# Performance work log

Measured on AMD Instinct MI355X. Metric: run time of the kernel, lower is better.

## Reference

```python
import jax, jax.numpy as jnp
import numpy as np

B, NPG, EPG = 128, 256, 2048   # graphs, nodes/graph, edges/graph
EMB, EH, L = 256, 64, 5
ATOM_V, BOND_V = 119, 16


def setup_inputs() -> dict:
    key = jax.random.key(0)
    ks = iter(jax.random.split(key, 32))
    s = 0.02
    inp = {
        'atom_idx': jax.random.randint(next(ks), (B, NPG), 0, ATOM_V),
        'local_edge_index': jax.random.randint(next(ks), (B, 2, EPG), 0, NPG),
        'edge_attr_idx': jax.random.randint(next(ks), (B, EPG), 0, BOND_V),
        'order': 3,
        'atom_emb': jax.random.normal(next(ks), (ATOM_V, EMB), jnp.float32) * s,
        'bond_emb_h': jax.random.normal(next(ks), (BOND_V, EH), jnp.float32) * s,
        'edge_lin_w': jax.random.normal(next(ks), (EH,), jnp.float32) * s,
        'edge_lin_b': jax.random.normal(next(ks), (1,), jnp.float32) * s,
        'bond_emb_l': jax.random.normal(next(ks), (L, BOND_V, EMB), jnp.float32) * s,
        'gin_eps': jnp.zeros((L,), jnp.float32),
        'mlp_w1': jax.random.normal(next(ks), (L, EMB, 2 * EMB), jnp.float32) * s,
        'mlp_b1': jax.random.normal(next(ks), (L, 2 * EMB), jnp.float32) * s,
        'mlp_bn_g': jnp.ones((L, 2 * EMB), jnp.float32),
        'mlp_bn_b': jnp.zeros((L, 2 * EMB), jnp.float32),
        'mlp_w2': jax.random.normal(next(ks), (L, 2 * EMB, EMB), jnp.float32) * s,
        'mlp_b2': jax.random.normal(next(ks), (L, EMB), jnp.float32) * s,
        'out_bn_g': jnp.ones((L, EMB), jnp.float32),
        'out_bn_b': jnp.zeros((L, EMB), jnp.float32),
        'vn_emb': jnp.zeros((1, EMB), jnp.float32),  # init constant 0 as in source
        'vn_w1': jax.random.normal(next(ks), (L - 1, EMB, 2 * EMB), jnp.float32) * s,
        'vn_b1': jax.random.normal(next(ks), (L - 1, 2 * EMB), jnp.float32) * s,
        'vn_w2': jax.random.normal(next(ks), (L - 1, 2 * EMB, EMB), jnp.float32) * s,
        'vn_b2': jax.random.normal(next(ks), (L - 1, EMB), jnp.float32) * s,
    }
    return inp


def _batchnorm(x, g, b):
    # training-mode BN math (biased variance), eps=1e-5 as in torch.nn.BatchNorm1d
    mu = x.mean(0)
    var = ((x - mu) ** 2).mean(0)
    return (x - mu) * jax.lax.rsqrt(var + 1e-5) * g + b


def reference(atom_idx, local_edge_index, edge_attr_idx, order,
              atom_emb, bond_emb_h, edge_lin_w, edge_lin_b, bond_emb_l, gin_eps,
              mlp_w1, mlp_b1, mlp_bn_g, mlp_bn_b, mlp_w2, mlp_b2,
              out_bn_g, out_bn_b, vn_emb, vn_w1, vn_b1, vn_w2, vn_b2):
    Bg, n = atom_idx.shape
    emb = atom_emb.shape[1]
    N = Bg * n
    nl = gin_eps.shape[0]

    # ---- per-graph learned-adjacency dense propagation (adj_learn=1) ----
    fea = atom_emb[atom_idx]                                       # [B,n,emb]
    ew = jax.nn.sigmoid(jnp.einsum('beh,h->be', bond_emb_h[edge_attr_idx], edge_lin_w)
                        + edge_lin_b[0])                           # [B,e]

    def per_graph(f, ei, w):
        adj = jnp.zeros((n, n), f.dtype).at[ei[0], ei[1]].set(w)
        adj = adj + jnp.eye(n, dtype=f.dtype)
        # A = diag(colsum^-1/2) @ adj @ diag(rowsum^-1/2)  (as in source naming)
        r_row = adj.sum(0) ** -0.5
        r_col = adj.sum(1) ** -0.5
        A = r_row[:, None] * adj * r_col[None, :]
        x = f
        y = f
        for _ in range(order):
            x = A @ x
            y = y + x
        return y / (order + 1.0)

    h = jax.vmap(per_graph)(fea, local_edge_index, ew).reshape(N, emb)

    # ---- flatten batched graph to global edge list ----
    batch = jnp.repeat(jnp.arange(Bg), n)                          # [N]
    off = (jnp.arange(Bg) * n)[:, None]
    src = (local_edge_index[:, 0] + off).reshape(-1)               # [E]
    dst = (local_edge_index[:, 1] + off).reshape(-1)
    ea = edge_attr_idx.reshape(-1)

    # ---- virtual-node GIN stack (eval: dropout = identity) ----
    vn = jnp.broadcast_to(vn_emb[0], (Bg, emb))
    for l in range(nl):
        h = h + vn[batch]
        h_in = h
        eemb = bond_emb_l[l][ea]                                   # [E,emb]
        msg = jax.nn.relu(h[src] + eemb)
        agg = jax.ops.segment_sum(msg, dst, num_segments=N)
        z = (1.0 + gin_eps[l]) * h + agg
        z = _batchnorm(z @ mlp_w1[l] + mlp_b1[l], mlp_bn_g[l], mlp_bn_b[l])
        z = jax.nn.relu(z) @ mlp_w2[l] + mlp_b2[l]
        z = _batchnorm(z, out_bn_g[l], out_bn_b[l])
        if l < nl - 1:
            z = jax.nn.relu(z)
            vt = jax.ops.segment_sum(h_in, batch, num_segments=Bg) + vn
            vn = jax.nn.relu(jax.nn.relu(vt @ vn_w1[l] + vn_b1[l]) @ vn_w2[l] + vn_b2[l])
        h = z
    return h  # JK='last'
```

## Files before the change

### kernel.cpp

```cpp
#include <hip/hip_runtime.h>
#include <math.h>


#define B_G   128
#define NPG   256
#define EPG   2048
#define EMB   256
#define NL    5
#define NNODE (B_G*NPG)
#define NEDGE (B_G*EPG)
#define FBUF  8388608

typedef __attribute__((ext_vector_type(8))) short bf16x8;
typedef __attribute__((ext_vector_type(4))) float f32x4;

__device__ __forceinline__ unsigned short round1(float x) {
  unsigned u = __builtin_bit_cast(unsigned, x);
  return (unsigned short)((u + 0x7FFFu + ((u >> 16) & 1u)) >> 16);
}

__device__ __forceinline__ float bdec(unsigned short h) {
  return __builtin_bit_cast(float, (unsigned)h << 16);
}

__device__ __forceinline__ void gload16(unsigned short* lds, const unsigned short* g) {
  __builtin_amdgcn_global_load_lds(
      (const __attribute__((address_space(1))) unsigned int*)g,
      (__attribute__((address_space(3))) unsigned int*)lds, 16, 0, 0);
}

__global__ void k_zero(uint4* p, int n16) {
  int i = blockIdx.x * 256 + threadIdx.x;
  if (i < n16) p[i] = make_uint4(0, 0, 0, 0);
}

__global__ void k_ewtbl(const float* __restrict__ bh, const float* __restrict__ w,
                        const float* __restrict__ b, float* __restrict__ tbl) {
  int v = threadIdx.x >> 6, t = threadIdx.x & 63;
  float p = bh[v * 64 + t] * w[t];
  for (int off = 32; off; off >>= 1) p += __shfl_down(p, off, 64);
  if (t == 0) tbl[v] = 1.0f / (1.0f + expf(-(p + b[0])));
}

__global__ void k_pack_adj(const int* __restrict__ lei, const int* __restrict__ ea,
                           int* __restrict__ packed) {
  int idx = blockIdx.x * 256 + threadIdx.x;
  int g = idx >> 11, e = idx & 2047;
  int s = lei[g * 4096 + e];
  int d = lei[g * 4096 + 2048 + e];
  int v = ((e + 1) << 4) | ea[g * 2048 + e];
  atomicMax(&packed[g * 65536 + s * 256 + d], v);
}

__global__ void k_unpack_adj(const int* __restrict__ packed,
                             const float* __restrict__ tbl, float* __restrict__ adj) {
  int idx = blockIdx.x * 256 + threadIdx.x;
  int v = packed[idx];
  int r = (idx >> 8) & 255, c = idx & 255;
  adj[idx] = (v ? tbl[v & 15] : 0.0f) + (r == c ? 1.0f : 0.0f);
}

__global__ __launch_bounds__(256)
void k_degsums(const float* __restrict__ adj, float* __restrict__ CSv,
               float* __restrict__ RCv) {
  int g = blockIdx.x, t = threadIdx.x;
  const float* Ag = adj + (size_t)g * 65536;
  float s0 = 0, s1 = 0, s2 = 0, s3 = 0;
  for (int i = 0; i < 256; i += 4) {
    s0 += Ag[(i + 0) * 256 + t]; s1 += Ag[(i + 1) * 256 + t];
    s2 += Ag[(i + 2) * 256 + t]; s3 += Ag[(i + 3) * 256 + t];
  }
  CSv[g * 256 + t] = rsqrtf((s0 + s1) + (s2 + s3));
  float4 r0 = make_float4(0, 0, 0, 0), r1 = r0, r2 = r0, r3 = r0;
  const float4* A4 = (const float4*)(Ag + t * 256);
  for (int j = 0; j < 64; j += 4) {
    float4 v0 = A4[j], v1 = A4[j + 1], v2 = A4[j + 2], v3 = A4[j + 3];
    r0.x += v0.x + v0.y; r0.y += v0.z + v0.w;
    r1.x += v1.x + v1.y; r1.y += v1.z + v1.w;
    r2.x += v2.x + v2.y; r2.y += v2.z + v2.w;
    r3.x += v3.x + v3.y; r3.y += v3.z + v3.w;
  }
  RCv[g * 256 + t] = rsqrtf((r0.x + r0.y) + (r1.x + r1.y) + (r2.x + r2.y) + (r3.x + r3.y));
}

__global__ void k_ascale(const float* __restrict__ adj, const float* __restrict__ CSv,
                         const float* __restrict__ RCv, unsigned short* __restrict__ Ahb) {
  int flat = blockIdx.x * 256 + threadIdx.x;
  int g = flat >> 14;
  int i = (flat >> 6) & 255, j4 = (flat & 63) * 4;
  size_t base = (size_t)g * 65536 + i * 256 + j4;
  float4 a = *(const float4*)&adj[base];
  float cs = CSv[g * 256 + i];
  float4 rc = *(const float4*)&RCv[g * 256 + j4];
  ushort4 o;
  o.x = round1(cs * a.x * rc.x); o.y = round1(cs * a.y * rc.y);
  o.z = round1(cs * a.z * rc.z); o.w = round1(cs * a.w * rc.w);
  *(ushort4*)&Ahb[base] = o;
}

__global__ void k_feaTb(const int* __restrict__ aidx, const float* __restrict__ aemb,
                        unsigned short* __restrict__ X0h) {
  int flat = blockIdx.x * 256 + threadIdx.x;
  int base = flat * 4;
  int g = base >> 16, e = (base >> 8) & 255, n0 = base & 255;
  const int* ai = &aidx[g * 256 + n0];
  ushort4 o;
  o.x = round1(aemb[ai[0] * 256 + e]);
  o.y = round1(aemb[ai[1] * 256 + e]);
  o.z = round1(aemb[ai[2] * 256 + e]);
  o.w = round1(aemb[ai[3] * 256 + e]);
  *(ushort4*)&X0h[base] = o;
}

__global__ __launch_bounds__(256)
void k_sumT(const unsigned short* __restrict__ X0, const unsigned short* __restrict__ X1,
            const unsigned short* __restrict__ X2, const unsigned short* __restrict__ X3,
            unsigned short* __restrict__ dst) {
  __shared__ float tl[64][65];
  size_t zo = (size_t)blockIdx.z * 65536;
  int n0 = blockIdx.x * 64, k0 = blockIdx.y * 64;
  int t = threadIdx.x;
  int c = (t & 15) * 4, r = t >> 4;
#pragma unroll
  for (int p = 0; p < 4; p++) {
    int rr = r + p * 16;
    size_t off = zo + (size_t)(k0 + rr) * 256 + n0 + c;
    ushort4 a = *(const ushort4*)&X0[off];
    ushort4 b = *(const ushort4*)&X1[off];
    ushort4 cc = *(const ushort4*)&X2[off];
    ushort4 d = *(const ushort4*)&X3[off];
    tl[rr][c + 0] = bdec(a.x) + bdec(b.x) + bdec(cc.x) + bdec(d.x);
    tl[rr][c + 1] = bdec(a.y) + bdec(b.y) + bdec(cc.y) + bdec(d.y);
    tl[rr][c + 2] = bdec(a.z) + bdec(b.z) + bdec(cc.z) + bdec(d.z);
    tl[rr][c + 3] = bdec(a.w) + bdec(b.w) + bdec(cc.w) + bdec(d.w);
  }
  __syncthreads();
#pragma unroll
  for (int p = 0; p < 4; p++) {
    int rr = r + p * 16;
    ushort4 o;
    o.x = round1(tl[c][rr] * 0.25f);     o.y = round1(tl[c + 1][rr] * 0.25f);
    o.z = round1(tl[c + 2][rr] * 0.25f); o.w = round1(tl[c + 3][rr] * 0.25f);
    *(ushort4*)&dst[zo + (size_t)(n0 + rr) * 256 + k0 + c] = o;
  }
}

__global__ __launch_bounds__(256)
void k_wtb(const float* __restrict__ src, unsigned short* __restrict__ dh,
           int K, int N, long ss, long sd) {
  __shared__ float tl[64][65];
  src += (size_t)blockIdx.z * ss;
  dh += (size_t)blockIdx.z * sd;
  int n0 = blockIdx.x * 64, k0 = blockIdx.y * 64;
  int t = threadIdx.x;
  int c = (t & 15) * 4, r = t >> 4;
#pragma unroll
  for (int p = 0; p < 4; p++) {
    int rr = r + p * 16;
    float4 v = *(const float4*)&src[(size_t)(k0 + rr) * N + n0 + c];
    tl[rr][c] = v.x; tl[rr][c + 1] = v.y; tl[rr][c + 2] = v.z; tl[rr][c + 3] = v.w;
  }
  __syncthreads();
#pragma unroll
  for (int p = 0; p < 4; p++) {
    int rr = r + p * 16;
    ushort4 hh;
    hh.x = round1(tl[c][rr]);     hh.y = round1(tl[c + 1][rr]);
    hh.z = round1(tl[c + 2][rr]); hh.w = round1(tl[c + 3][rr]);
    *(ushort4*)&dh[(size_t)(n0 + rr) * K + k0 + c] = hh;
  }
}

__global__ __launch_bounds__(256, 4)
void k_bgemm(const unsigned short* __restrict__ A_g, const unsigned short* __restrict__ B_g,
             const float* __restrict__ bias, float* __restrict__ Cf,
             unsigned short* __restrict__ Ch,
             float* __restrict__ Ssum, float* __restrict__ Ssq, int K, int N,
             long zA, long zB, long zC) {
  __shared__ alignas(16) unsigned short As[128 * 64];
  __shared__ alignas(16) unsigned short Bs[128 * 64];
  int z = blockIdx.z;
  A_g += (size_t)z * zA; B_g += (size_t)z * zB;
  if (Cf) Cf += (size_t)z * zC;
  if (Ch) Ch += (size_t)z * zC;
  int rowbase = blockIdx.y * 128, colbase = blockIdx.x * 128;
  int t = threadIdx.x, l = t & 63, wid = t >> 6;
  int wr = wid >> 1, wc = wid & 1;
  int r8 = l >> 3, cb = (l & 7) * 8;
  f32x4 acc[4][4];
#pragma unroll
  for (int i = 0; i < 4; i++)
#pragma unroll
    for (int j = 0; j < 4; j++) acc[i][j] = (f32x4){0, 0, 0, 0};

  for (int k0 = 0; k0 < K; k0 += 64) {
    __syncthreads();
#pragma unroll
    for (int i = 0; i < 4; i++) {
      int chunk = wid * 4 + i;
      int row = chunk * 8 + r8;
      gload16(As + chunk * 512, A_g + (size_t)(rowbase + row) * K + k0 + cb);
      gload16(Bs + chunk * 512, B_g + (size_t)(colbase + row) * K + k0 + cb);
    }
    __syncthreads();
#pragma unroll
    for (int ks = 0; ks < 2; ks++) {
      bf16x8 ah[4], bh[4];
#pragma unroll
      for (int fm = 0; fm < 4; fm++) {
        int r = wr * 64 + fm * 16 + (l & 15);
        ah[fm] = *(const bf16x8*)&As[r * 64 + ks * 32 + (l >> 4) * 8];
      }
#pragma unroll
      for (int fn = 0; fn < 4; fn++) {
        int c = wc * 64 + fn * 16 + (l & 15);
        bh[fn] = *(const bf16x8*)&Bs[c * 64 + ks * 32 + (l >> 4) * 8];
      }
#pragma unroll
      for (int fm = 0; fm < 4; fm++)
#pragma unroll
        for (int fn = 0; fn < 4; fn++)
          acc[fm][fn] = __builtin_amdgcn_mfma_f32_16x16x32_bf16(ah[fm], bh[fn], acc[fm][fn], 0, 0, 0);
    }
  }
  __syncthreads();
  float bi[4], scoll[4] = {0, 0, 0, 0}, qcoll[4] = {0, 0, 0, 0};
#pragma unroll
  for (int fn = 0; fn < 4; fn++)
    bi[fn] = bias ? bias[colbase + wc * 64 + fn * 16 + (l & 15)] : 0.0f;
#pragma unroll
  for (int fm = 0; fm < 4; fm++)
#pragma unroll
    for (int r4 = 0; r4 < 4; r4++) {
      int row = rowbase + wr * 64 + fm * 16 + (l >> 4) * 4 + r4;
#pragma unroll
      for (int fn = 0; fn < 4; fn++) {
        int col = colbase + wc * 64 + fn * 16 + (l & 15);
        float v = acc[fm][fn][r4] + bi[fn];
        size_t idx = (size_t)row * N + col;
        if (Cf) Cf[idx] = v;
        if (Ch) Ch[idx] = round1(v);
        scoll[fn] += v; qcoll[fn] += v * v;
      }
    }
  if (Ssum) {
    float* scr = (float*)As;
    scr[t] = 0.0f;
    __syncthreads();
#pragma unroll
    for (int fn = 0; fn < 4; fn++) {
      int cl_ = wc * 64 + fn * 16 + (l & 15);
      atomicAdd(&scr[cl_ * 2], scoll[fn]);
      atomicAdd(&scr[cl_ * 2 + 1], qcoll[fn]);
    }
    __syncthreads();
    if (t < 128) {
      atomicAdd(&Ssum[colbase + t], scr[t * 2]);
      atomicAdd(&Ssq[colbase + t], scr[t * 2 + 1]);
    }
  }
}

__global__ void k_bnsplit(unsigned short* __restrict__ Th,
                          const float* __restrict__ Ssum, const float* __restrict__ Ssq,
                          const float* __restrict__ g, const float* __restrict__ b) {
  size_t i = (size_t)blockIdx.x * 256 + threadIdx.x;
  int c4 = ((int)i & 127) * 4;
  ushort4 h4 = *(ushort4*)&Th[i * 4];
  float4 ss = *(const float4*)&Ssum[c4], qq = *(const float4*)&Ssq[c4];
  float4 gg = *(const float4*)&g[c4],    bb = *(const float4*)&b[c4];
  const float invN = 1.0f / 32768.0f;
  float x, mu, var, sc, sh;
#define BNS(cmp) \
  mu = ss.cmp * invN; var = qq.cmp * invN - mu * mu; \
  sc = rsqrtf(var + 1e-5f) * gg.cmp; sh = bb.cmp - mu * sc; \
  x = bdec(h4.cmp); x = fmaf(x, sc, sh); x = x > 0 ? x : 0; \
  h4.cmp = round1(x);
  BNS(x) BNS(y) BNS(z) BNS(w)
#undef BNS
  *(ushort4*)&Th[i * 4] = h4;
}

__global__ void k_count(const int* __restrict__ lei, int* __restrict__ counts) {
  int idx = blockIdx.x * 256 + threadIdx.x;
  int g = idx >> 11, e = idx & 2047;
  int d = lei[g * 4096 + 2048 + e];
  atomicAdd(&counts[g * 256 + d], 1);
}

__global__ void k_scan(const int* __restrict__ counts, int* __restrict__ rowptr,
                       int* __restrict__ pos) {
  int g = blockIdx.x, t = threadIdx.x;
  __shared__ int sc[256];
  int own = counts[g * 256 + t];
  sc[t] = own;
  __syncthreads();
  for (int off = 1; off < 256; off <<= 1) {
    int v = 0;
    if (t >= off) v = sc[t - off];
    __syncthreads();
    sc[t] += v;
    __syncthreads();
  }
  int val = g * 2048 + sc[t] - own;
  rowptr[g * 256 + t] = val;
  pos[g * 256 + t] = val;
  if (g == B_G - 1 && t == 255) rowptr[B_G * 256] = B_G * 2048;
}

__global__ void k_fill(const int* __restrict__ lei, const int* __restrict__ ea,
                       int* __restrict__ pos, int* __restrict__ csr) {
  int idx = blockIdx.x * 256 + threadIdx.x;
  int g = idx >> 11, e = idx & 2047;
  int s = lei[g * 4096 + e];
  int d = lei[g * 4096 + 2048 + e];
  int eav = ea[g * 2048 + e];
  int slot = atomicAdd(&pos[g * 256 + d], 1);
  csr[slot] = s | (eav << 16);
}

__global__ __launch_bounds__(256)
void k_agg(const unsigned short* __restrict__ H,
           const float* __restrict__ hsc, const float* __restrict__ hsh,
           const float* __restrict__ vn, int vns,
           const float* __restrict__ eemb,
           const int* __restrict__ rowptr, const int* __restrict__ csr,
           const float* __restrict__ geps, int l,
           unsigned short* __restrict__ Zh) {
  __shared__ float ee[16 * 256];
  for (int i = threadIdx.x; i < 4096; i += 256) ee[i] = eemb[i];
  __syncthreads();
  int lane = threadIdx.x & 63, w = threadIdx.x >> 6;
  int bid = (blockIdx.x & 7) * 1024 + (blockIdx.x >> 3);
  int m = bid * 4 + w;
  int g = m >> 8;
  int d = lane * 4;
  float eps1 = 1.0f + geps[l];
  float4 sc4 = make_float4(0, 0, 0, 0), sh4 = make_float4(0, 0, 0, 0);
  if (hsc) { sc4 = *(const float4*)&hsc[d]; sh4 = *(const float4*)&hsh[d]; }
  float4 vn4 = *(const float4*)&vn[(size_t)g * vns + d];
  int rp = rowptr[m], rp1 = rowptr[m + 1];
  float4 acc = make_float4(0, 0, 0, 0);
  int gbase = g << 8;
  for (int j = rp; j < rp1; j++) {
    int cw = csr[j];
    int src = cw & 0xFFFF, eav = cw >> 16;
    ushort4 hr = *(const ushort4*)&H[(size_t)(gbase + src) * 256 + d];
    float4 h4 = make_float4(bdec(hr.x), bdec(hr.y), bdec(hr.z), bdec(hr.w));
    if (hsc) {
      h4.x = fmaf(h4.x, sc4.x, sh4.x); h4.y = fmaf(h4.y, sc4.y, sh4.y);
      h4.z = fmaf(h4.z, sc4.z, sh4.z); h4.w = fmaf(h4.w, sc4.w, sh4.w);
      h4.x = h4.x > 0 ? h4.x : 0; h4.y = h4.y > 0 ? h4.y : 0;
      h4.z = h4.z > 0 ? h4.z : 0; h4.w = h4.w > 0 ? h4.w : 0;
    }
    const float4 e4 = *(const float4*)&ee[eav * 256 + d];
    float mx = h4.x + vn4.x + e4.x; float my = h4.y + vn4.y + e4.y;
    float mz = h4.z + vn4.z + e4.z; float mw = h4.w + vn4.w + e4.w;
    acc.x += mx > 0 ? mx : 0; acc.y += my > 0 ? my : 0;
    acc.z += mz > 0 ? mz : 0; acc.w += mw > 0 ? mw : 0;
  }
  ushort4 hsr = *(const ushort4*)&H[(size_t)m * 256 + d];
  float4 hs = make_float4(bdec(hsr.x), bdec(hsr.y), bdec(hsr.z), bdec(hsr.w));
  if (hsc) {
    hs.x = fmaf(hs.x, sc4.x, sh4.x); hs.y = fmaf(hs.y, sc4.y, sh4.y);
    hs.z = fmaf(hs.z, sc4.z, sh4.z); hs.w = fmaf(hs.w, sc4.w, sh4.w);
    hs.x = hs.x > 0 ? hs.x : 0; hs.y = hs.y > 0 ? hs.y : 0;
    hs.z = hs.z > 0 ? hs.z : 0; hs.w = hs.w > 0 ? hs.w : 0;
  }
  float4 z4;
  z4.x = eps1 * (hs.x + vn4.x) + acc.x;
  z4.y = eps1 * (hs.y + vn4.y) + acc.y;
  z4.z = eps1 * (hs.z + vn4.z) + acc.z;
  z4.w = eps1 * (hs.w + vn4.w) + acc.w;
  ushort4 hh;
  hh.x = round1(z4.x); hh.y = round1(z4.y);
  hh.z = round1(z4.z); hh.w = round1(z4.w);
  *(ushort4*)&Zh[(size_t)m * 256 + d] = hh;
}

__global__ __launch_bounds__(256)
void k_vnsum(const unsigned short* __restrict__ H,
             const float* __restrict__ hsc, const float* __restrict__ hsh,
             float* __restrict__ VNP) {
  int g = blockIdx.x >> 1, p = blockIdx.x & 1, t = threadIdx.x;
  float sc = 0, sh = 0;
  if (hsc) { sc = hsc[t]; sh = hsh[t]; }
  int base = g * 256 + p * 128;
  float s0 = 0, s1 = 0, s2 = 0, s3 = 0;
  for (int i = 0; i < 128; i += 4) {
    float v0 = bdec(H[(size_t)(base + i + 0) * 256 + t]);
    float v1 = bdec(H[(size_t)(base + i + 1) * 256 + t]);
    float v2 = bdec(H[(size_t)(base + i + 2) * 256 + t]);
    float v3 = bdec(H[(size_t)(base + i + 3) * 256 + t]);
    if (hsc) {
      v0 = fmaf(v0, sc, sh); v0 = v0 > 0 ? v0 : 0;
      v1 = fmaf(v1, sc, sh); v1 = v1 > 0 ? v1 : 0;
      v2 = fmaf(v2, sc, sh); v2 = v2 > 0 ? v2 : 0;
      v3 = fmaf(v3, sc, sh); v3 = v3 > 0 ? v3 : 0;
    }
    s0 += v0; s1 += v1; s2 += v2; s3 += v3;
  }
  VNP[(size_t)(p * 128 + g) * 256 + t] = (s0 + s1) + (s2 + s3);
}

__global__ __launch_bounds__(256)
void k_vn(const float* __restrict__ VNP,
          const float* __restrict__ vn_in, int vns,
          const float* __restrict__ W1, const float* __restrict__ B1,
          const float* __restrict__ W2, const float* __restrict__ B2,
          float* __restrict__ vn_out) {
  int g = blockIdx.x, t = threadIdx.x;
  __shared__ float vt[256];
  __shared__ float u[512];
  vt[t] = VNP[(size_t)g * 256 + t] + VNP[(size_t)(128 + g) * 256 + t]
        + 257.0f * vn_in[(size_t)g * vns + t];
  __syncthreads();
  for (int o = t; o < 512; o += 256) {
    float a = B1[o];
    for (int k = 0; k < 256; k++) a = fmaf(vt[k], W1[k * 512 + o], a);
    u[o] = a > 0 ? a : 0;
  }
  __syncthreads();
  float a = B2[t];
  for (int k = 0; k < 512; k++) a = fmaf(u[k], W2[k * 256 + t], a);
  vn_out[g * 256 + t] = a > 0 ? a : 0;
}

__global__ void k_bnfin(const float* __restrict__ Ssum, const float* __restrict__ Ssq,
                        const float* __restrict__ g, const float* __restrict__ b,
                        float* __restrict__ scale, float* __restrict__ shift,
                        int NC, float invN) {
  int c = blockIdx.x * 256 + threadIdx.x;
  if (c >= NC) return;
  float mu = Ssum[c] * invN;
  float var = Ssq[c] * invN - mu * mu;
  float rs = rsqrtf(var + 1e-5f);
  float s = rs * g[c];
  scale[c] = s;
  shift[c] = b[c] - mu * s;
}

__global__ void k_final(const float* __restrict__ T2, const float* __restrict__ sc,
                        const float* __restrict__ sh, float* __restrict__ out) {
  int i = blockIdx.x * 256 + threadIdx.x;
  int c4 = (i & 63) * 4;
  float4 v = *(const float4*)&T2[(size_t)i * 4];
  float4 s4 = *(const float4*)&sc[c4];
  float4 h4 = *(const float4*)&sh[c4];
  v.x = fmaf(v.x, s4.x, h4.x); v.y = fmaf(v.y, s4.y, h4.y);
  v.z = fmaf(v.z, s4.z, h4.z); v.w = fmaf(v.w, s4.w, h4.w);
  *(float4*)&out[(size_t)i * 4] = v;
}

extern "C" void kernel_launch(void* const* d_in, const int* in_sizes, int n_in,
                              void* d_out, int out_size, void* d_ws, size_t ws_size,
                              hipStream_t stream) {
  (void)in_sizes; (void)n_in; (void)out_size; (void)ws_size;
  const int*   atom_idx = (const int*)d_in[0];
  const int*   lei      = (const int*)d_in[1];
  const int*   eattr    = (const int*)d_in[2];
  const float* atom_emb = (const float*)d_in[4];
  const float* bemb_h   = (const float*)d_in[5];
  const float* elw      = (const float*)d_in[6];
  const float* elb      = (const float*)d_in[7];
  const float* bemb_l   = (const float*)d_in[8];
  const float* geps     = (const float*)d_in[9];
  const float* mw1      = (const float*)d_in[10];
  const float* mb1      = (const float*)d_in[11];
  const float* mbng     = (const float*)d_in[12];
  const float* mbnb     = (const float*)d_in[13];
  const float* mw2      = (const float*)d_in[14];
  const float* mb2      = (const float*)d_in[15];
  const float* obng     = (const float*)d_in[16];
  const float* obnb     = (const float*)d_in[17];
  const float* vne      = (const float*)d_in[18];
  const float* vw1      = (const float*)d_in[19];
  const float* vb1      = (const float*)d_in[20];
  const float* vw2      = (const float*)d_in[21];
  const float* vb2      = (const float*)d_in[22];
  float* out = (float*)d_out;

  float* W   = (float*)d_ws;
  float* A_  = W;
  float* U1  = W + (size_t)FBUF;
  float* U2  = W + (size_t)2 * FBUF;
  float* U3  = W + (size_t)3 * FBUF;
  float* Z_  = W + (size_t)4 * FBUF;
  float* SM  = W + (size_t)5 * FBUF;
  float* EWT = SM;
  float* S1S = SM + 256;
  float* S1Q = SM + 768;
  float* S2S = SM + 1280;
  float* S2Q = SM + 1536;
  float* SC2 = SM + 1792;
  float* SH2 = SM + 2048;
  float* VNA = SM + 2304;
  float* VNB = SM + 35072;
  float* CSv = SM + 67840;
  float* RCv = SM + 100608;
  int* ROWPTR = (int*)(SM + 133376);
  int* POS    = ROWPTR + 32772;
  int* COUNTS = POS + 32768;
  int* CSR    = COUNTS + 32768;
  unsigned short* W1hT = (unsigned short*)(SM + 493952);
  unsigned short* W2hT = (unsigned short*)(SM + 821632);
  float* T2f = A_;
  unsigned short* T2b = (unsigned short*)A_;
  unsigned short* H0b = (unsigned short*)U3;
  int* PACKED = (int*)U3;
  unsigned short* X0h = (unsigned short*)U1;
  unsigned short* X1h = X0h + 8388608;
  unsigned short* X2h = (unsigned short*)U2;
  unsigned short* X3h = X2h + 8388608;
  unsigned short* T1h = (unsigned short*)U1;
  unsigned short* Zh  = (unsigned short*)Z_;
  unsigned short* Ahb = (unsigned short*)(Z_ + (size_t)FBUF / 2);
  float* VNP  = (float*)POS;

  k_zero<<<8192, 256, 0, stream>>>((uint4*)PACKED, 2097152);
  k_zero<<<32, 256, 0, stream>>>((uint4*)COUNTS, 8192);
  k_ewtbl<<<1, 1024, 0, stream>>>(bemb_h, elw, elb, EWT);
  k_pack_adj<<<NEDGE / 256, 256, 0, stream>>>(lei, eattr, PACKED);
  k_unpack_adj<<<32768, 256, 0, stream>>>(PACKED, EWT, A_);
  k_degsums<<<B_G, 256, 0, stream>>>(A_, CSv, RCv);
  k_ascale<<<8192, 256, 0, stream>>>(A_, CSv, RCv, Ahb);
  k_wtb<<<dim3(8, 4, 5), 256, 0, stream>>>(mw1, W1hT, 256, 512, 131072, 131072);
  k_wtb<<<dim3(4, 8, 5), 256, 0, stream>>>(mw2, W2hT, 512, 256, 131072, 131072);
  k_feaTb<<<8192, 256, 0, stream>>>(atom_idx, atom_emb, X0h);
  k_bgemm<<<dim3(2, 2, B_G), 256, 0, stream>>>(X0h, Ahb, nullptr, nullptr, X1h,
      nullptr, nullptr, 256, 256, 65536, 65536, 65536);
  k_bgemm<<<dim3(2, 2, B_G), 256, 0, stream>>>(X1h, Ahb, nullptr, nullptr, X2h,
      nullptr, nullptr, 256, 256, 65536, 65536, 65536);
  k_bgemm<<<dim3(2, 2, B_G), 256, 0, stream>>>(X2h, Ahb, nullptr, nullptr, X3h,
      nullptr, nullptr, 256, 256, 65536, 65536, 65536);
  k_sumT<<<dim3(4, 4, B_G), 256, 0, stream>>>(X0h, X1h, X2h, X3h, H0b);

  k_count<<<NEDGE / 256, 256, 0, stream>>>(lei, COUNTS);
  k_scan<<<B_G, 256, 0, stream>>>(COUNTS, ROWPTR, POS);
  k_fill<<<NEDGE / 256, 256, 0, stream>>>(lei, eattr, POS, CSR);

  const float* vn_cur = vne; int vns = 0;
  float* vn_next = VNA;
  for (int l = 0; l < NL; l++) {
    const unsigned short* hsrc = (l == 0) ? H0b : T2b;
    const float* hsc  = (l == 0) ? nullptr : SC2;
    const float* hsh  = (l == 0) ? nullptr : SH2;
    k_agg<<<NNODE / 4, 256, 0, stream>>>(hsrc, hsc, hsh, vn_cur, vns,
        bemb_l + (size_t)l * 16 * EMB, ROWPTR, CSR, geps, l, Zh);
    if (l < NL - 1) {
      k_vnsum<<<256, 256, 0, stream>>>(hsrc, hsc, hsh, VNP);
      k_vn<<<B_G, 256, 0, stream>>>(VNP, vn_cur, vns,
          vw1 + (size_t)l * EMB * 512, vb1 + (size_t)l * 512,
          vw2 + (size_t)l * 512 * EMB, vb2 + (size_t)l * EMB, vn_next);
    }
    k_zero<<<2, 256, 0, stream>>>((uint4*)S1S, 384);
    k_bgemm<<<dim3(4, 256, 1), 256, 0, stream>>>(Zh,
        W1hT + (size_t)l * 131072, mb1 + (size_t)l * 512,
        nullptr, T1h, S1S, S1Q, 256, 512, 0, 0, 0);
    k_bnsplit<<<16384, 256, 0, stream>>>(T1h, S1S, S1Q,
        mbng + (size_t)l * 512, mbnb + (size_t)l * 512);
    if (l < NL - 1)
      k_bgemm<<<dim3(2, 256, 1), 256, 0, stream>>>(T1h,
          W2hT + (size_t)l * 131072, mb2 + (size_t)l * 256,
          nullptr, T2b, S2S, S2Q, 512, 256, 0, 0, 0);
    else
      k_bgemm<<<dim3(2, 256, 1), 256, 0, stream>>>(T1h,
          W2hT + (size_t)l * 131072, mb2 + (size_t)l * 256,
          T2f, nullptr, S2S, S2Q, 512, 256, 0, 0, 0);
    k_bnfin<<<1, 256, 0, stream>>>(S2S, S2Q, obng + (size_t)l * EMB,
        obnb + (size_t)l * EMB, SC2, SH2, 256, 1.0f / NNODE);
    if (l < NL - 1) {
      vn_cur = vn_next; vns = EMB;
      vn_next = (vn_next == VNA) ? VNB : VNA;
    }
  }
  k_final<<<8192, 256, 0, stream>>>(T2f, SC2, SH2, out);
}
```

Measured before the change: 1.028 ms.

## Fuse BN+ReLU into second MLP GEMM A-load; restructure aggregation with prefetch

Removes the standalone k_bnsplit pass. The first-layer BN scale and shift are now computed by k_bnfin, and BN plus ReLU is applied while loading A tiles into shared memory in the second GEMM. This avoids a full read-modify-write of the 32768x512 bf16 intermediate on every layer. The aggregation kernel now processes four nodes per wave with a one-ahead software prefetch of the CSR entry and neighbour row, and stores the edge embeddings as bf16 in LDS. The costs are a synchronous (non-async) A-load path in the GEMM, an extra bf16 rounding of the edge embeddings, and fewer blocks for the aggregation.

```diff
diff --git a/kernel.cpp b/kernel.cpp
--- a/kernel.cpp
+++ b/kernel.cpp
@@ -176,7 +176,8 @@
              const float* __restrict__ bias, float* __restrict__ Cf,
              unsigned short* __restrict__ Ch,
              float* __restrict__ Ssum, float* __restrict__ Ssq, int K, int N,
-             long zA, long zB, long zC) {
+             long zA, long zB, long zC,
+             const float* __restrict__ ascale, const float* __restrict__ ashift) {
   __shared__ alignas(16) unsigned short As[128 * 64];
   __shared__ alignas(16) unsigned short Bs[128 * 64];
   int z = blockIdx.z;
@@ -195,12 +196,38 @@
 
   for (int k0 = 0; k0 < K; k0 += 64) {
     __syncthreads();
-#pragma unroll
-    for (int i = 0; i < 4; i++) {
-      int chunk = wid * 4 + i;
-      int row = chunk * 8 + r8;
-      gload16(As + chunk * 512, A_g + (size_t)(rowbase + row) * K + k0 + cb);
-      gload16(Bs + chunk * 512, B_g + (size_t)(colbase + row) * K + k0 + cb);
+    if (ascale) {
+      float4 s0 = *(const float4*)&ascale[k0 + cb];
+      float4 s1 = *(const float4*)&ascale[k0 + cb + 4];
+      float4 h0 = *(const float4*)&ashift[k0 + cb];
+      float4 h1 = *(const float4*)&ashift[k0 + cb + 4];
+#pragma unroll
+      for (int i = 0; i < 4; i++) {
+        int chunk = wid * 4 + i;
+        int row = chunk * 8 + r8;
+        const unsigned short* src = A_g + (size_t)(rowbase + row) * K + k0 + cb;
+        ushort4 v0 = *(const ushort4*)src;
+        ushort4 v1 = *(const ushort4*)(src + 4);
+        float x;
+        ushort4 o0, o1;
+#define BNF(dst, u, s, h) x = fmaf(bdec(u), s, h); x = x > 0 ? x : 0; dst = round1(x);
+        BNF(o0.x, v0.x, s0.x, h0.x) BNF(o0.y, v0.y, s0.y, h0.y)
+        BNF(o0.z, v0.z, s0.z, h0.z) BNF(o0.w, v0.w, s0.w, h0.w)
+        BNF(o1.x, v1.x, s1.x, h1.x) BNF(o1.y, v1.y, s1.y, h1.y)
+        BNF(o1.z, v1.z, s1.z, h1.z) BNF(o1.w, v1.w, s1.w, h1.w)
+#undef BNF
+        *(ushort4*)&As[chunk * 512 + l * 8] = o0;
+        *(ushort4*)&As[chunk * 512 + l * 8 + 4] = o1;
+        gload16(Bs + chunk * 512, B_g + (size_t)(colbase + row) * K + k0 + cb);
+      }
+    } else {
+#pragma unroll
+      for (int i = 0; i < 4; i++) {
+        int chunk = wid * 4 + i;
+        int row = chunk * 8 + r8;
+        gload16(As + chunk * 512, A_g + (size_t)(rowbase + row) * K + k0 + cb);
+        gload16(Bs + chunk * 512, B_g + (size_t)(colbase + row) * K + k0 + cb);
+      }
     }
     __syncthreads();
 #pragma unroll
@@ -259,26 +286,6 @@
       atomicAdd(&Ssq[colbase + t], scr[t * 2 + 1]);
     }
   }
-}
-
-__global__ void k_bnsplit(unsigned short* __restrict__ Th,
-                          const float* __restrict__ Ssum, const float* __restrict__ Ssq,
-                          const float* __restrict__ g, const float* __restrict__ b) {
-  size_t i = (size_t)blockIdx.x * 256 + threadIdx.x;
-  int c4 = ((int)i & 127) * 4;
-  ushort4 h4 = *(ushort4*)&Th[i * 4];
-  float4 ss = *(const float4*)&Ssum[c4], qq = *(const float4*)&Ssq[c4];
-  float4 gg = *(const float4*)&g[c4],    bb = *(const float4*)&b[c4];
-  const float invN = 1.0f / 32768.0f;
-  float x, mu, var, sc, sh;
-#define BNS(cmp) \
-  mu = ss.cmp * invN; var = qq.cmp * invN - mu * mu; \
-  sc = rsqrtf(var + 1e-5f) * gg.cmp; sh = bb.cmp - mu * sc; \
-  x = bdec(h4.cmp); x = fmaf(x, sc, sh); x = x > 0 ? x : 0; \
-  h4.cmp = round1(x);
-  BNS(x) BNS(y) BNS(z) BNS(w)
-#undef BNS
-  *(ushort4*)&Th[i * 4] = h4;
 }
 
 __global__ void k_count(const int* __restrict__ lei, int* __restrict__ counts) {
@@ -327,55 +334,67 @@
            const int* __restrict__ rowptr, const int* __restrict__ csr,
            const float* __restrict__ geps, int l,
            unsigned short* __restrict__ Zh) {
-  __shared__ float ee[16 * 256];
-  for (int i = threadIdx.x; i < 4096; i += 256) ee[i] = eemb[i];
+  __shared__ unsigned short ee[16 * 256];
+  for (int i = threadIdx.x; i < 4096; i += 256) ee[i] = round1(eemb[i]);
   __syncthreads();
   int lane = threadIdx.x & 63, w = threadIdx.x >> 6;
-  int bid = (blockIdx.x & 7) * 1024 + (blockIdx.x >> 3);
-  int m = bid * 4 + w;
-  int g = m >> 8;
+  int bid = (blockIdx.x & 7) * 256 + (blockIdx.x >> 3);
+  int g = bid >> 4;
   int d = lane * 4;
   float eps1 = 1.0f + geps[l];
   float4 sc4 = make_float4(0, 0, 0, 0), sh4 = make_float4(0, 0, 0, 0);
   if (hsc) { sc4 = *(const float4*)&hsc[d]; sh4 = *(const float4*)&hsh[d]; }
   float4 vn4 = *(const float4*)&vn[(size_t)g * vns + d];
-  int rp = rowptr[m], rp1 = rowptr[m + 1];
-  float4 acc = make_float4(0, 0, 0, 0);
   int gbase = g << 8;
-  for (int j = rp; j < rp1; j++) {
-    int cw = csr[j];
-    int src = cw & 0xFFFF, eav = cw >> 16;
-    ushort4 hr = *(const ushort4*)&H[(size_t)(gbase + src) * 256 + d];
-    float4 h4 = make_float4(bdec(hr.x), bdec(hr.y), bdec(hr.z), bdec(hr.w));
+#pragma unroll 1
+  for (int mi = 0; mi < 4; mi++) {
+    int m = bid * 16 + w * 4 + mi;
+    int rp = rowptr[m], rp1 = rowptr[m + 1];
+    ushort4 hsr = *(const ushort4*)&H[(size_t)m * 256 + d];
+    float4 acc = make_float4(0, 0, 0, 0);
+    int cw = 0; ushort4 hr = make_ushort4(0, 0, 0, 0);
+    if (rp < rp1) {
+      cw = csr[rp];
+      hr = *(const ushort4*)&H[(size_t)(gbase + (cw & 0xFFFF)) * 256 + d];
+    }
+    for (int j = rp; j < rp1; j++) {
+      int cwn = 0; ushort4 hrn = make_ushort4(0, 0, 0, 0);
+      if (j + 1 < rp1) {
+        cwn = csr[j + 1];
+        hrn = *(const ushort4*)&H[(size_t)(gbase + (cwn & 0xFFFF)) * 256 + d];
+      }
+      int eav = cw >> 16;
+      float4 h4 = make_float4(bdec(hr.x), bdec(hr.y), bdec(hr.z), bdec(hr.w));
+      if (hsc) {
+        h4.x = fmaf(h4.x, sc4.x, sh4.x); h4.y = fmaf(h4.y, sc4.y, sh4.y);
+        h4.z = fmaf(h4.z, sc4.z, sh4.z); h4.w = fmaf(h4.w, sc4.w, sh4.w);
+        h4.x = h4.x > 0 ? h4.x : 0; h4.y = h4.y > 0 ? h4.y : 0;
+        h4.z = h4.z > 0 ? h4.z : 0; h4.w = h4.w > 0 ? h4.w : 0;
+      }
+      const ushort4 er = *(const ushort4*)&ee[eav * 256 + d];
+      float mx = h4.x + vn4.x + bdec(er.x); float my = h4.y + vn4.y + bdec(er.y);
+      float mz = h4.z + vn4.z + bdec(er.z); float mw = h4.w + vn4.w + bdec(er.w);
+      acc.x += mx > 0 ? mx : 0; acc.y += my > 0 ? my : 0;
+      acc.z += mz > 0 ? mz : 0; acc.w += mw > 0 ? mw : 0;
+      cw = cwn; hr = hrn;
+    }
+    float4 hs = make_float4(bdec(hsr.x), bdec(hsr.y), bdec(hsr.z), bdec(hsr.w));
     if (hsc) {
-      h4.x = fmaf(h4.x, sc4.x, sh4.x); h4.y = fmaf(h4.y, sc4.y, sh4.y);
-      h4.z = fmaf(h4.z, sc4.z, sh4.z); h4.w = fmaf(h4.w, sc4.w, sh4.w);
-      h4.x = h4.x > 0 ? h4.x : 0; h4.y = h4.y > 0 ? h4.y : 0;
-      h4.z = h4.z > 0 ? h4.z : 0; h4.w = h4.w > 0 ? h4.w : 0;
-    }
-    const float4 e4 = *(const float4*)&ee[eav * 256 + d];
-    float mx = h4.x + vn4.x + e4.x; float my = h4.y + vn4.y + e4.y;
-    float mz = h4.z + vn4.z + e4.z; float mw = h4.w + vn4.w + e4.w;
-    acc.x += mx > 0 ? mx : 0; acc.y += my > 0 ? my : 0;
-    acc.z += mz > 0 ? mz : 0; acc.w += mw > 0 ? mw : 0;
-  }
-  ushort4 hsr = *(const ushort4*)&H[(size_t)m * 256 + d];
-  float4 hs = make_float4(bdec(hsr.x), bdec(hsr.y), bdec(hsr.z), bdec(hsr.w));
-  if (hsc) {
-    hs.x = fmaf(hs.x, sc4.x, sh4.x); hs.y = fmaf(hs.y, sc4.y, sh4.y);
-    hs.z = fmaf(hs.z, sc4.z, sh4.z); hs.w = fmaf(hs.w, sc4.w, sh4.w);
-    hs.x = hs.x > 0 ? hs.x : 0; hs.y = hs.y > 0 ? hs.y : 0;
-    hs.z = hs.z > 0 ? hs.z : 0; hs.w = hs.w > 0 ? hs.w : 0;
-  }
-  float4 z4;
-  z4.x = eps1 * (hs.x + vn4.x) + acc.x;
-  z4.y = eps1 * (hs.y + vn4.y) + acc.y;
-  z4.z = eps1 * (hs.z + vn4.z) + acc.z;
-  z4.w = eps1 * (hs.w + vn4.w) + acc.w;
-  ushort4 hh;
-  hh.x = round1(z4.x); hh.y = round1(z4.y);
-  hh.z = round1(z4.z); hh.w = round1(z4.w);
-  *(ushort4*)&Zh[(size_t)m * 256 + d] = hh;
+      hs.x = fmaf(hs.x, sc4.x, sh4.x); hs.y = fmaf(hs.y, sc4.y, sh4.y);
+      hs.z = fmaf(hs.z, sc4.z, sh4.z); hs.w = fmaf(hs.w, sc4.w, sh4.w);
+      hs.x = hs.x > 0 ? hs.x : 0; hs.y = hs.y > 0 ? hs.y : 0;
+      hs.z = hs.z > 0 ? hs.z : 0; hs.w = hs.w > 0 ? hs.w : 0;
+    }
+    float4 z4;
+    z4.x = eps1 * (hs.x + vn4.x) + acc.x;
+    z4.y = eps1 * (hs.y + vn4.y) + acc.y;
+    z4.z = eps1 * (hs.z + vn4.z) + acc.z;
+    z4.w = eps1 * (hs.w + vn4.w) + acc.w;
+    ushort4 hh;
+    hh.x = round1(z4.x); hh.y = round1(z4.y);
+    hh.z = round1(z4.z); hh.w = round1(z4.w);
+    *(ushort4*)&Zh[(size_t)m * 256 + d] = hh;
+  }
 }
 
 __global__ __launch_bounds__(256)
@@ -494,16 +513,18 @@
   float* S2Q = SM + 1536;
   float* SC2 = SM + 1792;
   float* SH2 = SM + 2048;
-  float* VNA = SM + 2304;
-  float* VNB = SM + 35072;
-  float* CSv = SM + 67840;
-  float* RCv = SM + 100608;
-  int* ROWPTR = (int*)(SM + 133376);
+  float* SC1 = SM + 2304;
+  float* SH1 = SM + 2816;
+  float* VNA = SM + 3328;
+  float* VNB = SM + 36096;
+  float* CSv = SM + 68864;
+  float* RCv = SM + 101632;
+  int* ROWPTR = (int*)(SM + 134400);
   int* POS    = ROWPTR + 32772;
   int* COUNTS = POS + 32768;
   int* CSR    = COUNTS + 32768;
-  unsigned short* W1hT = (unsigned short*)(SM + 493952);
-  unsigned short* W2hT = (unsigned short*)(SM + 821632);
+  unsigned short* W1hT = (unsigned short*)(SM + 494852);
+  unsigned short* W2hT = (unsigned short*)(SM + 822532);
   float* T2f = A_;
   unsigned short* T2b = (unsigned short*)A_;
   unsigned short* H0b = (unsigned short*)U3;
@@ -528,11 +549,11 @@
   k_wtb<<<dim3(4, 8, 5), 256, 0, stream>>>(mw2, W2hT, 512, 256, 131072, 131072);
   k_feaTb<<<8192, 256, 0, stream>>>(atom_idx, atom_emb, X0h);
   k_bgemm<<<dim3(2, 2, B_G), 256, 0, stream>>>(X0h, Ahb, nullptr, nullptr, X1h,
-      nullptr, nullptr, 256, 256, 65536, 65536, 65536);
+      nullptr, nullptr, 256, 256, 65536, 65536, 65536, nullptr, nullptr);
   k_bgemm<<<dim3(2, 2, B_G), 256, 0, stream>>>(X1h, Ahb, nullptr, nullptr, X2h,
-      nullptr, nullptr, 256, 256, 65536, 65536, 65536);
+      nullptr, nullptr, 256, 256, 65536, 65536, 65536, nullptr, nullptr);
   k_bgemm<<<dim3(2, 2, B_G), 256, 0, stream>>>(X2h, Ahb, nullptr, nullptr, X3h,
-      nullptr, nullptr, 256, 256, 65536, 65536, 65536);
+      nullptr, nullptr, 256, 256, 65536, 65536, 65536, nullptr, nullptr);
   k_sumT<<<dim3(4, 4, B_G), 256, 0, stream>>>(X0h, X1h, X2h, X3h, H0b);
 
   k_count<<<NEDGE / 256, 256, 0, stream>>>(lei, COUNTS);
@@ -545,7 +566,7 @@
     const unsigned short* hsrc = (l == 0) ? H0b : T2b;
     const float* hsc  = (l == 0) ? nullptr : SC2;
     const float* hsh  = (l == 0) ? nullptr : SH2;
-    k_agg<<<NNODE / 4, 256, 0, stream>>>(hsrc, hsc, hsh, vn_cur, vns,
+    k_agg<<<2048, 256, 0, stream>>>(hsrc, hsc, hsh, vn_cur, vns,
         bemb_l + (size_t)l * 16 * EMB, ROWPTR, CSR, geps, l, Zh);
     if (l < NL - 1) {
       k_vnsum<<<256, 256, 0, stream>>>(hsrc, hsc, hsh, VNP);
@@ -556,17 +577,17 @@
     k_zero<<<2, 256, 0, stream>>>((uint4*)S1S, 384);
     k_bgemm<<<dim3(4, 256, 1), 256, 0, stream>>>(Zh,
         W1hT + (size_t)l * 131072, mb1 + (size_t)l * 512,
-        nullptr, T1h, S1S, S1Q, 256, 512, 0, 0, 0);
-    k_bnsplit<<<16384, 256, 0, stream>>>(T1h, S1S, S1Q,
-        mbng + (size_t)l * 512, mbnb + (size_t)l * 512);
+        nullptr, T1h, S1S, S1Q, 256, 512, 0, 0, 0, nullptr, nullptr);
+    k_bnfin<<<2, 256, 0, stream>>>(S1S, S1Q, mbng + (size_t)l * 512,
+        mbnb + (size_t)l * 512, SC1, SH1, 512, 1.0f / NNODE);
     if (l < NL - 1)
       k_bgemm<<<dim3(2, 256, 1), 256, 0, stream>>>(T1h,
           W2hT + (size_t)l * 131072, mb2 + (size_t)l * 256,
-          nullptr, T2b, S2S, S2Q, 512, 256, 0, 0, 0);
+          nullptr, T2b, S2S, S2Q, 512, 256, 0, 0, 0, SC1, SH1);
     else
       k_bgemm<<<dim3(2, 256, 1), 256, 0, stream>>>(T1h,
           W2hT + (size_t)l * 131072, mb2 + (size_t)l * 256,
-          T2f, nullptr, S2S, S2Q, 512, 256, 0, 0, 0);
+          T2f, nullptr, S2S, S2Q, 512, 256, 0, 0, 0, SC1, SH1);
     k_bnfin<<<1, 256, 0, stream>>>(S2S, S2Q, obng + (size_t)l * EMB,
         obnb + (size_t)l * EMB, SC2, SH2, 256, 1.0f / NNODE);
     if (l < NL - 1) {
```

Result: slower. 1.105 ms (+7.5%).
